# Performance work log

Hardware: AMD Instinct MI355X
Metric: run time of the kernel (lower is better)

## Reference

```python
import jax, jax.numpy as jnp
import numpy as np

N, DIM, HID = 100000, 128, 256


def setup_inputs() -> dict:
    key = jax.random.key(0)
    ks = jax.random.split(key, 12)
    def lin(kw, kb, out_f, in_f):
        bound = 1.0 / np.sqrt(in_f)
        W = jax.random.uniform(kw, (out_f, in_f), jnp.float32, -bound, bound)
        b = jax.random.uniform(kb, (out_f,), jnp.float32, -bound, bound)
        return W, b
    x = jax.random.normal(ks[0], (N, DIM), jnp.float32)
    adj_col = jax.random.uniform(ks[1], (N,), jnp.float32)
    W_n2e, b_n2e = lin(ks[2], ks[3], HID, 2 * DIM)
    W_e2e, b_e2e = lin(ks[4], ks[5], HID, HID)
    W_e2n, b_e2n = lin(ks[6], ks[7], HID, HID)
    W_out, b_out = lin(ks[8], ks[9], DIM, DIM + HID)
    return {"x": x, "adj_col": adj_col, "i": 7,
            "W_n2e": W_n2e, "b_n2e": b_n2e,
            "W_e2e": W_e2e, "b_e2e": b_e2e,
            "W_e2n": W_e2n, "b_e2n": b_e2n,
            "W_out": W_out, "b_out": b_out}


def reference(x, adj_col, i, W_n2e, b_n2e, W_e2e, b_e2e, W_e2n, b_e2n, W_out, b_out):
    # gather node i and broadcast to all N nodes, concat with all node feats
    xi = x[i]                                        # [dim]
    ender = jnp.broadcast_to(xi, x.shape)            # [N, dim]
    h = jnp.concatenate([x, ender], axis=1)          # [N, 2*dim]
    # edge MLP: two linear+relu
    h = jax.nn.relu(h @ W_n2e.T + b_n2e)             # [N, hid]
    h = jax.nn.relu(h @ W_e2e.T + b_e2e)             # [N, hid]
    # adjacency-masked sum over nodes
    h = jnp.sum(h * adj_col[:, None], axis=0)        # [hid]
    # node update MLP + residual
    h = h @ W_e2n.T + b_e2n                          # [hid]
    out = jnp.concatenate([xi, h], axis=-1) @ W_out.T + b_out  # [dim]
    return xi + out
```

## Files before the change

kernel.cpp:

```cpp
#include <hip/hip_runtime.h>


#define DIM 128
#define HID 256
#define BM 64
#define TPB 512

typedef float  f32x4 __attribute__((ext_vector_type(4)));
typedef short  s16x8 __attribute__((ext_vector_type(8)));

__device__ __forceinline__ unsigned short f2bf(float f) {
    unsigned u = __float_as_uint(f);
    return (unsigned short)((u + 0x7FFFu + ((u >> 16) & 1u)) >> 16);
}
__device__ __forceinline__ float bf2f(unsigned short h) {
    return __uint_as_float(((unsigned)h) << 16);
}

#define MFMA_BF16(acc, a, b) \
    asm volatile("v_mfma_f32_16x16x32_bf16 %0, %1, %2, %0" \
                 : "+v"(acc) : "v"(a), "v"(b))

#define XH_OFF   0
#define XL_OFF   16384
#define H1H_OFF  32768
#define H1L_OFF  65536
#define ADJ_OFF  98304
#define SM_BYTES 98560

__global__ void prep_c1(const float* __restrict__ x,
                        const int* __restrict__ ip,
                        const float* __restrict__ W_n2e,
                        const float* __restrict__ b_n2e,
                        float* __restrict__ c1) {
    int o = blockIdx.x;
    int lane = threadIdx.x;
    const float* xi = x + (size_t)(*ip) * DIM;
    const float* wr = W_n2e + (size_t)o * (2 * DIM) + DIM;
    float s = wr[lane] * xi[lane] + wr[lane + 64] * xi[lane + 64];
    #pragma unroll
    for (int off = 32; off > 0; off >>= 1) s += __shfl_down(s, off);
    if (lane == 0) c1[o] = s + b_n2e[o];
}

__global__ void prep_pack(const float* __restrict__ Wn2e,
                          const float* __restrict__ We2e,
                          short* __restrict__ W1h, short* __restrict__ W1l,
                          short* __restrict__ W2h, short* __restrict__ W2l) {
    int tid = blockIdx.x * 256 + threadIdx.x;
    float w; int o, k; short *dh, *dl;
    if (tid < 32768) {
        o = tid >> 7; k = tid & 127;
        w = Wn2e[(size_t)o * 256 + k];
        dh = W1h; dl = W1l;
    } else {
        int u = tid - 32768;
        o = u >> 8; k = u & 255;
        w = We2e[(size_t)o * 256 + k];
        dh = W2h; dl = W2l;
    }
    int ks = k >> 5, koff = k & 31;
    int lane = ((koff >> 3) << 4) | (o & 15);
    int cb = o >> 4;
    size_t dst = ((size_t)((ks * 16 + cb) * 64 + lane)) * 8 + (koff & 7);
    unsigned short h = f2bf(w);
    dh[dst] = (short)h;
    dl[dst] = (short)f2bf(w - bf2f(h));
}

__global__ __launch_bounds__(TPB, 1)
void main_kernel(const float* __restrict__ x,
                 const float* __restrict__ adj,
                 const short* __restrict__ W1h, const short* __restrict__ W1l,
                 const short* __restrict__ W2h, const short* __restrict__ W2l,
                 const float* __restrict__ c1, const float* __restrict__ b2,
                 float* __restrict__ P, int n_nodes, int ntiles) {
    __shared__ __attribute__((aligned(16))) unsigned char sm[SM_BYTES];

    const int t  = threadIdx.x;
    const int l  = t & 63;
    const int w  = __builtin_amdgcn_readfirstlane(t >> 6);
    const int lc = l & 15;
    const int lg = l >> 4;

    float c1v[2], b2v[2];
    #pragma unroll
    for (int nf = 0; nf < 2; ++nf) {
        int col = w * 32 + nf * 16 + lc;
        c1v[nf] = c1[col];
        b2v[nf] = b2[col];
    }

    float spart[2] = {0.f, 0.f};
    const float4* xg4 = (const float4*)x;

    for (int tile = blockIdx.x; tile < ntiles; tile += gridDim.x) {
        const int bn = tile * BM;

        __syncthreads();

        #pragma unroll
        for (int j = 0; j < 4; ++j) {
            int f  = t + j * TPB;
            int r  = f >> 5;
            int c4 = f & 31;
            int node = bn + r;
            float4 v = (node < n_nodes) ? xg4[(size_t)node * 32 + c4]
                                        : make_float4(0.f, 0.f, 0.f, 0.f);
            unsigned short h0 = f2bf(v.x), h1 = f2bf(v.y),
                           h2 = f2bf(v.z), h3 = f2bf(v.w);
            uint2 hu, lu;
            hu.x = (unsigned)h0 | ((unsigned)h1 << 16);
            hu.y = (unsigned)h2 | ((unsigned)h3 << 16);
            lu.x = (unsigned)f2bf(v.x - bf2f(h0)) |
                   ((unsigned)f2bf(v.y - bf2f(h1)) << 16);
            lu.y = (unsigned)f2bf(v.z - bf2f(h2)) |
                   ((unsigned)f2bf(v.w - bf2f(h3)) << 16);
            int cb = (c4 * 8) ^ ((r & 7) << 4);
            *(uint2*)(sm + XH_OFF + r * 256 + cb) = hu;
            *(uint2*)(sm + XL_OFF + r * 256 + cb) = lu;
        }
        if (t < BM) {
            int node = bn + t;
            *(float*)(sm + ADJ_OFF + t * 4) = (node < n_nodes) ? adj[node] : 0.f;
        }
        __syncthreads();

        f32x4 acc1[4][2];
        #pragma unroll
        for (int mf = 0; mf < 4; ++mf)
            #pragma unroll
            for (int nf = 0; nf < 2; ++nf)
                acc1[mf][nf] = (f32x4){0.f, 0.f, 0.f, 0.f};

        #pragma unroll
        for (int ks = 0; ks < 4; ++ks) {
            s16x8 ah[4], al[4];
            #pragma unroll
            for (int mf = 0; mf < 4; ++mf) {
                int row = mf * 16 + lc;
                int cb = (ks * 64 + lg * 16) ^ ((row & 7) << 4);
                ah[mf] = *(const s16x8*)(sm + XH_OFF + row * 256 + cb);
                al[mf] = *(const s16x8*)(sm + XL_OFF + row * 256 + cb);
            }
            s16x8 bh[2], bl[2];
            #pragma unroll
            for (int nf = 0; nf < 2; ++nf) {
                size_t bidx = ((size_t)((ks * 16 + (w * 2 + nf)) * 64 + l)) * 8;
                bh[nf] = *(const s16x8*)(W1h + bidx);
                bl[nf] = *(const s16x8*)(W1l + bidx);
            }
            #pragma unroll
            for (int mf = 0; mf < 4; ++mf)
                #pragma unroll
                for (int nf = 0; nf < 2; ++nf) {
                    MFMA_BF16(acc1[mf][nf], ah[mf], bh[nf]);
                    MFMA_BF16(acc1[mf][nf], al[mf], bh[nf]);
                    MFMA_BF16(acc1[mf][nf], ah[mf], bl[nf]);
                }
        }

        __syncthreads();
        asm volatile("s_nop 7\n\ts_nop 7\n\ts_nop 7" ::: );

        #pragma unroll
        for (int mf = 0; mf < 4; ++mf)
            #pragma unroll
            for (int nf = 0; nf < 2; ++nf) {
                int col = w * 32 + nf * 16 + lc;
                #pragma unroll
                for (int r = 0; r < 4; ++r) {
                    int row = mf * 16 + lg * 4 + r;
                    float v = fmaxf(acc1[mf][nf][r] + c1v[nf], 0.f);
                    unsigned short h = f2bf(v);
                    unsigned short lo = f2bf(v - bf2f(h));
                    int cb = (col * 2) ^ ((row & 7) << 4);
                    *(unsigned short*)(sm + H1H_OFF + row * 512 + cb) = h;
                    *(unsigned short*)(sm + H1L_OFF + row * 512 + cb) = lo;
                }
            }
        __syncthreads();

        f32x4 acc2[4][2];
        #pragma unroll
        for (int mf = 0; mf < 4; ++mf)
            #pragma unroll
            for (int nf = 0; nf < 2; ++nf)
                acc2[mf][nf] = (f32x4){0.f, 0.f, 0.f, 0.f};

        #pragma unroll
        for (int ks = 0; ks < 8; ++ks) {
            s16x8 ah[4], al[4];
            #pragma unroll
            for (int mf = 0; mf < 4; ++mf) {
                int row = mf * 16 + lc;
                int cb = (ks * 64 + lg * 16) ^ ((row & 7) << 4);
                ah[mf] = *(const s16x8*)(sm + H1H_OFF + row * 512 + cb);
                al[mf] = *(const s16x8*)(sm + H1L_OFF + row * 512 + cb);
            }
            s16x8 bh[2], bl[2];
            #pragma unroll
            for (int nf = 0; nf < 2; ++nf) {
                size_t bidx = ((size_t)((ks * 16 + (w * 2 + nf)) * 64 + l)) * 8;
                bh[nf] = *(const s16x8*)(W2h + bidx);
                bl[nf] = *(const s16x8*)(W2l + bidx);
            }
            #pragma unroll
            for (int mf = 0; mf < 4; ++mf)
                #pragma unroll
                for (int nf = 0; nf < 2; ++nf) {
                    MFMA_BF16(acc2[mf][nf], ah[mf], bh[nf]);
                    MFMA_BF16(acc2[mf][nf], al[mf], bh[nf]);
                    MFMA_BF16(acc2[mf][nf], ah[mf], bl[nf]);
                }
        }

        asm volatile("s_nop 7\n\ts_nop 7\n\ts_nop 7" ::: );

        #pragma unroll
        for (int mf = 0; mf < 4; ++mf)
            #pragma unroll
            for (int r = 0; r < 4; ++r) {
                int row = mf * 16 + lg * 4 + r;
                float adv = *(const float*)(sm + ADJ_OFF + row * 4);
                #pragma unroll
                for (int nf = 0; nf < 2; ++nf)
                    spart[nf] += fmaxf(acc2[mf][nf][r] + b2v[nf], 0.f) * adv;
            }
    }

    #pragma unroll
    for (int nf = 0; nf < 2; ++nf) {
        float s = spart[nf];
        s += __shfl_xor(s, 16);
        s += __shfl_xor(s, 32);
        if (l < 16)
            P[(size_t)blockIdx.x * HID + w * 32 + nf * 16 + l] = s;
    }
}

__global__ void tail1(const float* __restrict__ P, float* __restrict__ Q,
                      int rows_per) {
    int b = blockIdx.x;
    int t = threadIdx.x;
    float s = 0.f;
    for (int j = 0; j < rows_per; ++j)
        s += P[(size_t)(b * rows_per + j) * HID + t];
    Q[(size_t)b * HID + t] = s;
}

__global__ void tail2(const float* __restrict__ x,
                      const int* __restrict__ ip,
                      const float* __restrict__ Q,
                      const float* __restrict__ W_e2n,
                      const float* __restrict__ b_e2n,
                      const float* __restrict__ W_out,
                      const float* __restrict__ b_out,
                      float* __restrict__ out) {
    __shared__ float gs[HID];
    __shared__ float hs[HID];
    __shared__ float xis[DIM];
    int t = threadIdx.x;
    const float* xi = x + (size_t)(*ip) * DIM;
    if (t < DIM) xis[t] = xi[t];
    float s = 0.f;
    #pragma unroll 8
    for (int b = 0; b < 64; ++b) s += Q[(size_t)b * HID + t];
    gs[t] = s;
    __syncthreads();
    {
        const float* wr = W_e2n + (size_t)t * HID;
        float h = b_e2n[t];
        #pragma unroll 8
        for (int k = 0; k < HID; ++k) h = fmaf(wr[k], gs[k], h);
        hs[t] = h;
    }
    __syncthreads();
    if (t < DIM) {
        const float* wo = W_out + (size_t)t * (DIM + HID);
        float v = b_out[t];
        #pragma unroll 8
        for (int k = 0; k < DIM; ++k) v = fmaf(wo[k], xis[k], v);
        #pragma unroll 8
        for (int k = 0; k < HID; ++k) v = fmaf(wo[DIM + k], hs[k], v);
        out[t] = xis[t] + v;
    }
}

extern "C" void kernel_launch(void* const* d_in, const int* in_sizes, int n_in,
                              void* d_out, int out_size, void* d_ws, size_t ws_size,
                              hipStream_t stream) {
    const float* x     = (const float*)d_in[0];
    const float* adj   = (const float*)d_in[1];
    const int*   ip    = (const int*)d_in[2];
    const float* W_n2e = (const float*)d_in[3];
    const float* b_n2e = (const float*)d_in[4];
    const float* W_e2e = (const float*)d_in[5];
    const float* b_e2e = (const float*)d_in[6];
    const float* W_e2n = (const float*)d_in[7];
    const float* b_e2n = (const float*)d_in[8];
    const float* W_out = (const float*)d_in[9];
    const float* b_out = (const float*)d_in[10];
    float* out = (float*)d_out;

    const int n_nodes = in_sizes[1];
    const int ntiles  = (n_nodes + BM - 1) / BM;

    short* W1h = (short*)d_ws;
    short* W1l = W1h + 32768;
    short* W2h = W1l + 32768;
    short* W2l = W2h + 65536;
    float* c1  = (float*)(W2l + 65536);
    float* Q   = c1 + HID;
    float* P   = Q + 64 * HID;

    const size_t fixed_bytes = 196608 * sizeof(short) + (HID + 64 * HID) * sizeof(float);
    int nb = 512;
    while (nb > 64 && fixed_bytes + (size_t)nb * HID * sizeof(float) > ws_size)
        nb >>= 1;

    prep_c1<<<HID, 64, 0, stream>>>(x, ip, W_n2e, b_n2e, c1);
    prep_pack<<<384, 256, 0, stream>>>(W_n2e, W_e2e, W1h, W1l, W2h, W2l);
    main_kernel<<<nb, TPB, 0, stream>>>(x, adj, W1h, W1l, W2h, W2l, c1, b_e2e,
                                        P, n_nodes, ntiles);
    tail1<<<64, HID, 0, stream>>>(P, Q, nb / 64);
    tail2<<<1, HID, 0, stream>>>(x, ip, Q, W_e2n, b_e2n, W_out, b_out, out);
}
```

Baseline: 213.5 us.

## Fuse prep kernels and tail reduction into main kernel, prefetch weights, shrink LDS

Merges the two prep kernels into one launch and folds both tail reduction kernels into the main kernel using a last-block-done atomic counter. The H1 staging buffers now alias the X staging region, cutting shared memory from about 98KB to 66KB, and launch bounds rise to allow more blocks per CU. Weight fragments are double-buffered from global memory one k-step ahead, and the MFMAs are reordered into independent groups. This removes launch overhead and serial tail kernels, at the cost of a single-block final reduction over 512 partials and atomic traffic.

```diff
diff --git a/kernel.cpp b/kernel.cpp
--- a/kernel.cpp
+++ b/kernel.cpp
@@ -3,8 +3,9 @@
 
 #define DIM 128
 #define HID 256
-#define BM 64
+#define BM  64
 #define TPB 512
+#define NB  512
 
 typedef float  f32x4 __attribute__((ext_vector_type(4)));
 typedef short  s16x8 __attribute__((ext_vector_type(8)));
@@ -23,30 +24,30 @@
 
 #define XH_OFF   0
 #define XL_OFF   16384
-#define H1H_OFF  32768
-#define H1L_OFF  65536
-#define ADJ_OFF  98304
-#define SM_BYTES 98560
-
-__global__ void prep_c1(const float* __restrict__ x,
-                        const int* __restrict__ ip,
-                        const float* __restrict__ W_n2e,
-                        const float* __restrict__ b_n2e,
-                        float* __restrict__ c1) {
-    int o = blockIdx.x;
-    int lane = threadIdx.x;
-    const float* xi = x + (size_t)(*ip) * DIM;
-    const float* wr = W_n2e + (size_t)o * (2 * DIM) + DIM;
-    float s = wr[lane] * xi[lane] + wr[lane + 64] * xi[lane + 64];
-    #pragma unroll
-    for (int off = 32; off > 0; off >>= 1) s += __shfl_down(s, off);
-    if (lane == 0) c1[o] = s + b_n2e[o];
-}
-
-__global__ void prep_pack(const float* __restrict__ Wn2e,
-                          const float* __restrict__ We2e,
-                          short* __restrict__ W1h, short* __restrict__ W1l,
-                          short* __restrict__ W2h, short* __restrict__ W2l) {
+#define H1H_OFF  0
+#define H1L_OFF  32768
+#define ADJ_OFF  65536
+#define SM_BYTES 65792
+
+__global__ void prep_kernel(const float* __restrict__ x,
+                            const int* __restrict__ ip,
+                            const float* __restrict__ Wn2e,
+                            const float* __restrict__ bn2e,
+                            const float* __restrict__ We2e,
+                            short* __restrict__ W1h, short* __restrict__ W1l,
+                            short* __restrict__ W2h, short* __restrict__ W2l,
+                            float* __restrict__ c1, int* __restrict__ cnt) {
+    if (blockIdx.x == 384) {
+        int o = threadIdx.x;
+        const float* xi = x + (size_t)(*ip) * DIM;
+        const float* wr = Wn2e + (size_t)o * (2 * DIM) + DIM;
+        float s = bn2e[o];
+        #pragma unroll 8
+        for (int k = 0; k < DIM; ++k) s = fmaf(wr[k], xi[k], s);
+        c1[o] = s;
+        if (o == 0) *cnt = 0;
+        return;
+    }
     int tid = blockIdx.x * 256 + threadIdx.x;
     float w; int o, k; short *dh, *dl;
     if (tid < 32768) {
@@ -68,14 +69,19 @@
     dl[dst] = (short)f2bf(w - bf2f(h));
 }
 
-__global__ __launch_bounds__(TPB, 1)
+__global__ __launch_bounds__(TPB, 4)
 void main_kernel(const float* __restrict__ x,
                  const float* __restrict__ adj,
+                 const int* __restrict__ ip,
                  const short* __restrict__ W1h, const short* __restrict__ W1l,
                  const short* __restrict__ W2h, const short* __restrict__ W2l,
                  const float* __restrict__ c1, const float* __restrict__ b2,
-                 float* __restrict__ P, int n_nodes, int ntiles) {
+                 const float* __restrict__ W_e2n, const float* __restrict__ b_e2n,
+                 const float* __restrict__ W_out, const float* __restrict__ b_out,
+                 float* __restrict__ P, int* __restrict__ cnt,
+                 float* __restrict__ out, int n_nodes, int ntiles) {
     __shared__ __attribute__((aligned(16))) unsigned char sm[SM_BYTES];
+    __shared__ int lastFlag;
 
     const int t  = threadIdx.x;
     const int l  = t & 63;
@@ -90,6 +96,11 @@
         c1v[nf] = c1[col];
         b2v[nf] = b2[col];
     }
+
+    const s16x8* pW1h = (const s16x8*)W1h + (size_t)(w * 2) * 64 + l;
+    const s16x8* pW1l = (const s16x8*)W1l + (size_t)(w * 2) * 64 + l;
+    const s16x8* pW2h = (const s16x8*)W2h + (size_t)(w * 2) * 64 + l;
+    const s16x8* pW2l = (const s16x8*)W2l + (size_t)(w * 2) * 64 + l;
 
     float spart[2] = {0.f, 0.f};
     const float4* xg4 = (const float4*)x;
@@ -126,38 +137,49 @@
         }
         __syncthreads();
 
-        f32x4 acc1[4][2];
+        f32x4 acc[4][2];
         #pragma unroll
         for (int mf = 0; mf < 4; ++mf)
             #pragma unroll
             for (int nf = 0; nf < 2; ++nf)
-                acc1[mf][nf] = (f32x4){0.f, 0.f, 0.f, 0.f};
-
-        #pragma unroll
-        for (int ks = 0; ks < 4; ++ks) {
-            s16x8 ah[4], al[4];
-            #pragma unroll
-            for (int mf = 0; mf < 4; ++mf) {
-                int row = mf * 16 + lc;
-                int cb = (ks * 64 + lg * 16) ^ ((row & 7) << 4);
-                ah[mf] = *(const s16x8*)(sm + XH_OFF + row * 256 + cb);
-                al[mf] = *(const s16x8*)(sm + XL_OFF + row * 256 + cb);
+                acc[mf][nf] = (f32x4){0.f, 0.f, 0.f, 0.f};
+
+        {
+            s16x8 bh[2][2], bl[2][2];
+            bh[0][0] = pW1h[0];  bh[0][1] = pW1h[64];
+            bl[0][0] = pW1l[0];  bl[0][1] = pW1l[64];
+            #pragma unroll
+            for (int ks = 0; ks < 4; ++ks) {
+                int cur = ks & 1, nxt = cur ^ 1;
+                if (ks < 3) {
+                    size_t off = (size_t)(ks + 1) * 1024;
+                    bh[nxt][0] = pW1h[off];  bh[nxt][1] = pW1h[off + 64];
+                    bl[nxt][0] = pW1l[off];  bl[nxt][1] = pW1l[off + 64];
+                }
+                s16x8 ah[4], al[4];
+                #pragma unroll
+                for (int mf = 0; mf < 4; ++mf) {
+                    int row = mf * 16 + lc;
+                    int cb = (ks * 64 + lg * 16) ^ ((row & 7) << 4);
+                    ah[mf] = *(const s16x8*)(sm + XH_OFF + row * 256 + cb);
+                    al[mf] = *(const s16x8*)(sm + XL_OFF + row * 256 + cb);
+                }
+                #pragma unroll
+                for (int mf = 0; mf < 4; ++mf) {
+                    MFMA_BF16(acc[mf][0], ah[mf], bh[cur][0]);
+                    MFMA_BF16(acc[mf][1], ah[mf], bh[cur][1]);
+                }
+                #pragma unroll
+                for (int mf = 0; mf < 4; ++mf) {
+                    MFMA_BF16(acc[mf][0], al[mf], bh[cur][0]);
+                    MFMA_BF16(acc[mf][1], al[mf], bh[cur][1]);
+                }
+                #pragma unroll
+                for (int mf = 0; mf < 4; ++mf) {
+                    MFMA_BF16(acc[mf][0], ah[mf], bl[cur][0]);
+                    MFMA_BF16(acc[mf][1], ah[mf], bl[cur][1]);
+                }
             }
-            s16x8 bh[2], bl[2];
-            #pragma unroll
-            for (int nf = 0; nf < 2; ++nf) {
-                size_t bidx = ((size_t)((ks * 16 + (w * 2 + nf)) * 64 + l)) * 8;
-                bh[nf] = *(const s16x8*)(W1h + bidx);
-                bl[nf] = *(const s16x8*)(W1l + bidx);
-            }
-            #pragma unroll
-            for (int mf = 0; mf < 4; ++mf)
-                #pragma unroll
-                for (int nf = 0; nf < 2; ++nf) {
-                    MFMA_BF16(acc1[mf][nf], ah[mf], bh[nf]);
-                    MFMA_BF16(acc1[mf][nf], al[mf], bh[nf]);
-                    MFMA_BF16(acc1[mf][nf], ah[mf], bl[nf]);
-                }
         }
 
         __syncthreads();
@@ -171,7 +193,7 @@
                 #pragma unroll
                 for (int r = 0; r < 4; ++r) {
                     int row = mf * 16 + lg * 4 + r;
-                    float v = fmaxf(acc1[mf][nf][r] + c1v[nf], 0.f);
+                    float v = fmaxf(acc[mf][nf][r] + c1v[nf], 0.f);
                     unsigned short h = f2bf(v);
                     unsigned short lo = f2bf(v - bf2f(h));
                     int cb = (col * 2) ^ ((row & 7) << 4);
@@ -181,38 +203,48 @@
             }
         __syncthreads();
 
-        f32x4 acc2[4][2];
         #pragma unroll
         for (int mf = 0; mf < 4; ++mf)
             #pragma unroll
             for (int nf = 0; nf < 2; ++nf)
-                acc2[mf][nf] = (f32x4){0.f, 0.f, 0.f, 0.f};
-
-        #pragma unroll
-        for (int ks = 0; ks < 8; ++ks) {
-            s16x8 ah[4], al[4];
-            #pragma unroll
-            for (int mf = 0; mf < 4; ++mf) {
-                int row = mf * 16 + lc;
-                int cb = (ks * 64 + lg * 16) ^ ((row & 7) << 4);
-                ah[mf] = *(const s16x8*)(sm + H1H_OFF + row * 512 + cb);
-                al[mf] = *(const s16x8*)(sm + H1L_OFF + row * 512 + cb);
+                acc[mf][nf] = (f32x4){0.f, 0.f, 0.f, 0.f};
+
+        {
+            s16x8 bh[2][2], bl[2][2];
+            bh[0][0] = pW2h[0];  bh[0][1] = pW2h[64];
+            bl[0][0] = pW2l[0];  bl[0][1] = pW2l[64];
+            #pragma unroll
+            for (int ks = 0; ks < 8; ++ks) {
+                int cur = ks & 1, nxt = cur ^ 1;
+                if (ks < 7) {
+                    size_t off = (size_t)(ks + 1) * 1024;
+                    bh[nxt][0] = pW2h[off];  bh[nxt][1] = pW2h[off + 64];
+                    bl[nxt][0] = pW2l[off];  bl[nxt][1] = pW2l[off + 64];
+                }
+                s16x8 ah[4], al[4];
+                #pragma unroll
+                for (int mf = 0; mf < 4; ++mf) {
+                    int row = mf * 16 + lc;
+                    int cb = (ks * 64 + lg * 16) ^ ((row & 7) << 4);
+                    ah[mf] = *(const s16x8*)(sm + H1H_OFF + row * 512 + cb);
+                    al[mf] = *(const s16x8*)(sm + H1L_OFF + row * 512 + cb);
+                }
+                #pragma unroll
+                for (int mf = 0; mf < 4; ++mf) {
+                    MFMA_BF16(acc[mf][0], ah[mf], bh[cur][0]);
+                    MFMA_BF16(acc[mf][1], ah[mf], bh[cur][1]);
+                }
+                #pragma unroll
+                for (int mf = 0; mf < 4; ++mf) {
+                    MFMA_BF16(acc[mf][0], al[mf], bh[cur][0]);
+                    MFMA_BF16(acc[mf][1], al[mf], bh[cur][1]);
+                }
+                #pragma unroll
+                for (int mf = 0; mf < 4; ++mf) {
+                    MFMA_BF16(acc[mf][0], ah[mf], bl[cur][0]);
+                    MFMA_BF16(acc[mf][1], ah[mf], bl[cur][1]);
+                }
             }
-            s16x8 bh[2], bl[2];
-            #pragma unroll
-            for (int nf = 0; nf < 2; ++nf) {
-                size_t bidx = ((size_t)((ks * 16 + (w * 2 + nf)) * 64 + l)) * 8;
-                bh[nf] = *(const s16x8*)(W2h + bidx);
-                bl[nf] = *(const s16x8*)(W2l + bidx);
-            }
-            #pragma unroll
-            for (int mf = 0; mf < 4; ++mf)
-                #pragma unroll
-                for (int nf = 0; nf < 2; ++nf) {
-                    MFMA_BF16(acc2[mf][nf], ah[mf], bh[nf]);
-                    MFMA_BF16(acc2[mf][nf], al[mf], bh[nf]);
-                    MFMA_BF16(acc2[mf][nf], ah[mf], bl[nf]);
-                }
         }
 
         asm volatile("s_nop 7\n\ts_nop 7\n\ts_nop 7" ::: );
@@ -225,7 +257,7 @@
                 float adv = *(const float*)(sm + ADJ_OFF + row * 4);
                 #pragma unroll
                 for (int nf = 0; nf < 2; ++nf)
-                    spart[nf] += fmaxf(acc2[mf][nf][r] + b2v[nf], 0.f) * adv;
+                    spart[nf] += fmaxf(acc[mf][nf][r] + b2v[nf], 0.f) * adv;
             }
     }
 
@@ -235,55 +267,43 @@
         s += __shfl_xor(s, 16);
         s += __shfl_xor(s, 32);
         if (l < 16)
-            P[(size_t)blockIdx.x * HID + w * 32 + nf * 16 + l] = s;
-    }
-}
-
-__global__ void tail1(const float* __restrict__ P, float* __restrict__ Q,
-                      int rows_per) {
-    int b = blockIdx.x;
-    int t = threadIdx.x;
-    float s = 0.f;
-    for (int j = 0; j < rows_per; ++j)
-        s += P[(size_t)(b * rows_per + j) * HID + t];
-    Q[(size_t)b * HID + t] = s;
-}
-
-__global__ void tail2(const float* __restrict__ x,
-                      const int* __restrict__ ip,
-                      const float* __restrict__ Q,
-                      const float* __restrict__ W_e2n,
-                      const float* __restrict__ b_e2n,
-                      const float* __restrict__ W_out,
-                      const float* __restrict__ b_out,
-                      float* __restrict__ out) {
-    __shared__ float gs[HID];
-    __shared__ float hs[HID];
-    __shared__ float xis[DIM];
-    int t = threadIdx.x;
-    const float* xi = x + (size_t)(*ip) * DIM;
-    if (t < DIM) xis[t] = xi[t];
-    float s = 0.f;
-    #pragma unroll 8
-    for (int b = 0; b < 64; ++b) s += Q[(size_t)b * HID + t];
-    gs[t] = s;
+            atomicExch(&P[(size_t)blockIdx.x * HID + w * 32 + nf * 16 + l], s);
+    }
+
+    __threadfence();
+    if (t == 0) lastFlag = (atomicAdd(cnt, 1) == (int)gridDim.x - 1);
     __syncthreads();
+    if (!lastFlag) return;
+    __threadfence();
+
+    float* smf = (float*)sm;
     {
+        float s = 0.f;
+        int o = t & 255, half = t >> 8;
+        for (int b = half; b < (int)gridDim.x; b += 2)
+            s += atomicAdd(&P[(size_t)b * HID + o], 0.f);
+        smf[t] = s;
+    }
+    __syncthreads();
+    if (t < HID) smf[t] += smf[t + HID];
+    __syncthreads();
+    if (t < HID) {
         const float* wr = W_e2n + (size_t)t * HID;
         float h = b_e2n[t];
         #pragma unroll 8
-        for (int k = 0; k < HID; ++k) h = fmaf(wr[k], gs[k], h);
-        hs[t] = h;
+        for (int k = 0; k < HID; ++k) h = fmaf(wr[k], smf[k], h);
+        smf[HID + t] = h;
     }
     __syncthreads();
     if (t < DIM) {
+        const float* xi = x + (size_t)(*ip) * DIM;
         const float* wo = W_out + (size_t)t * (DIM + HID);
-        float v = b_out[t];
+        float v = b_out[t] + xi[t];
         #pragma unroll 8
-        for (int k = 0; k < DIM; ++k) v = fmaf(wo[k], xis[k], v);
+        for (int k = 0; k < DIM; ++k) v = fmaf(wo[k], xi[k], v);
         #pragma unroll 8
-        for (int k = 0; k < HID; ++k) v = fmaf(wo[DIM + k], hs[k], v);
-        out[t] = xis[t] + v;
+        for (int k = 0; k < HID; ++k) v = fmaf(wo[DIM + k], smf[HID + k], v);
+        out[t] = v;
     }
 }
 
@@ -311,18 +331,12 @@
     short* W2h = W1l + 32768;
     short* W2l = W2h + 65536;
     float* c1  = (float*)(W2l + 65536);
-    float* Q   = c1 + HID;
-    float* P   = Q + 64 * HID;
-
-    const size_t fixed_bytes = 196608 * sizeof(short) + (HID + 64 * HID) * sizeof(float);
-    int nb = 512;
-    while (nb > 64 && fixed_bytes + (size_t)nb * HID * sizeof(float) > ws_size)
-        nb >>= 1;
-
-    prep_c1<<<HID, 64, 0, stream>>>(x, ip, W_n2e, b_n2e, c1);
-    prep_pack<<<384, 256, 0, stream>>>(W_n2e, W_e2e, W1h, W1l, W2h, W2l);
-    main_kernel<<<nb, TPB, 0, stream>>>(x, adj, W1h, W1l, W2h, W2l, c1, b_e2e,
-                                        P, n_nodes, ntiles);
-    tail1<<<64, HID, 0, stream>>>(P, Q, nb / 64);
-    tail2<<<1, HID, 0, stream>>>(x, ip, Q, W_e2n, b_e2n, W_out, b_out, out);
-}
+    float* P   = c1 + HID;
+    int*   cnt = (int*)(P + (size_t)NB * HID);
+
+    prep_kernel<<<385, 256, 0, stream>>>(x, ip, W_n2e, b_n2e, W_e2e,
+                                         W1h, W1l, W2h, W2l, c1, cnt);
+    main_kernel<<<NB, TPB, 0, stream>>>(x, adj, ip, W1h, W1l, W2h, W2l,
+                                        c1, b_e2e, W_e2n, b_e2n, W_out, b_out,
+                                        P, cnt, out, n_nodes, ntiles);
+}
```

Result: slower. 467.0 us (+118.7%).
